# Kernel optimization log

Measured on AMD Instinct MI355X. Metric: run time of the kernel, lower is better.

The kernel has to match this reference:

```python
import jax, jax.numpy as jnp
import numpy as np

IN_CAPS, OUT_CAPS, OUT_DIM = 32, 10, 16


def squash(s):
    # s: [B, out_caps, out_dim]
    sq = jnp.sum(s * s, axis=2)              # [B, out_caps]
    mod = jnp.sqrt(sq)
    scale = sq / (1.0 + sq) / mod            # matches torch: sqrmod/(1+sqrmod)/mod
    return scale[..., None] * s


def setup_inputs() -> dict:
    key = jax.random.key(0)
    k1, k2 = jax.random.split(key)
    B, in_dim = 4096, 288
    caps_output = jax.random.normal(k1, (B, IN_CAPS, in_dim), dtype=jnp.float32)
    # W initialized uniform(-1/32, 1/32) in the original; scale randn similarly small
    W = jax.random.uniform(k2, (IN_CAPS, in_dim, OUT_CAPS * OUT_DIM),
                           dtype=jnp.float32, minval=-1.0 / 32, maxval=1.0 / 32)
    b = jnp.zeros((IN_CAPS, OUT_CAPS), dtype=jnp.float32)
    return {"caps_output": caps_output, "W": W, "b": b}


def reference(caps_output, W, b):
    B = caps_output.shape[0]
    # caps_output.unsqueeze(2).matmul(W): per-input-capsule matmul
    u = jnp.einsum('bni,nio->bno', caps_output, W)          # [B, 32, 160]
    u = u.reshape(B, IN_CAPS, OUT_CAPS, OUT_DIM)            # [B, 32, 10, 16]

    c = jax.nn.softmax(b, axis=1)                           # [32, 10]
    s = jnp.einsum('no,bnod->bod', c, u)                    # [B, 10, 16]
    v = squash(s)

    b_batch = jnp.broadcast_to(b, (B, IN_CAPS, OUT_CAPS))
    for _ in range(3):
        # agreement: <u_predict, v>
        b_batch = b_batch + jnp.einsum('bnod,bod->bno', u, v)
        c = jax.nn.softmax(b_batch, axis=-1)                # [B, 32, 10]
        s = jnp.einsum('bno,bnod->bod', c, u)
        v = squash(s)
    return v
```

## Files before the change

kernel.cpp:

```cpp
#include <hip/hip_runtime.h>
#include <hip/hip_bf16.h>

#define IN_CAPS 32
#define OUT_CAPS 10
#define NOUT 160
#define KDIM 288
#define BATCH 4096
#define KSTEPS 9
#define CTILES 10
#define STR2 162

typedef __bf16 bf16x8 __attribute__((ext_vector_type(8)));
typedef float  f32x4  __attribute__((ext_vector_type(4)));
typedef __attribute__((address_space(1))) void as1_t;
typedef __attribute__((address_space(3))) void as3_t;

__global__ __launch_bounds__(256) void prep_w(const float* __restrict__ W,
                                              __bf16* __restrict__ Wf) {
    int f = blockIdx.x * 256 + threadIdx.x;
    int j    = f & 7;
    int l    = (f >> 3) & 63;
    int rest = f >> 9;
    int c    = rest % CTILES;
    int tnk  = rest / CTILES;
    int ks   = tnk % KSTEPS;
    int n    = tnk / KSTEPS;
    int k    = ks * 32 + (l >> 4) * 8 + j;
    int col  = c * 16 + (l & 15);
    Wf[f] = (__bf16)W[(n * KDIM + k) * NOUT + col];
}

__global__ __launch_bounds__(256) void gemm_u(const float* __restrict__ caps,
                                              const __bf16* __restrict__ Wf,
                                              uint4* __restrict__ up) {
    __shared__ float abuf[3][64 * 32];

    const int n    = blockIdx.y;
    const int rb   = blockIdx.x;
    const int w    = threadIdx.x >> 6;
    const int lane = threadIdx.x & 63;
    const int lm   = lane & 15;
    const int lk   = lane >> 4;

    const int s0 = w * 128 + lane;
    const int s1 = s0 + 64;
    const int r0 = s0 >> 3;
    const int r1 = s1 >> 3;
    const int c0 = (s0 & 7) ^ (r0 & 7);
    const int c1 = (s1 & 7) ^ (r1 & 7);
    const float* g0 = caps + (size_t)(rb * 64 + r0) * (IN_CAPS * KDIM) + n * KDIM + c0 * 4;
    const float* g1 = caps + (size_t)(rb * 64 + r1) * (IN_CAPS * KDIM) + n * KDIM + c1 * 4;

    f32x4 acc[CTILES];
#pragma unroll
    for (int ct = 0; ct < CTILES; ++ct) acc[ct] = (f32x4){0.f, 0.f, 0.f, 0.f};

    const int rloc = w * 16 + lm;
    const int h0   = ((lk * 2)     ^ (lm & 7)) * 4;
    const int h1   = ((lk * 2 + 1) ^ (lm & 7)) * 4;
    const __bf16* wfn = Wf + (size_t)n * (KSTEPS * CTILES * 512) + lane * 8;

    __builtin_amdgcn_global_load_lds((const as1_t*)g0, (as3_t*)&abuf[0][w * 512],       16, 0, 0);
    __builtin_amdgcn_global_load_lds((const as1_t*)g1, (as3_t*)&abuf[0][w * 512 + 256], 16, 0, 0);
    __builtin_amdgcn_global_load_lds((const as1_t*)(g0 + 32), (as3_t*)&abuf[1][w * 512],       16, 0, 0);
    __builtin_amdgcn_global_load_lds((const as1_t*)(g1 + 32), (as3_t*)&abuf[1][w * 512 + 256], 16, 0, 0);

#pragma unroll
    for (int ks = 0; ks < KSTEPS; ++ks) {
        if (ks + 1 < KSTEPS) asm volatile("s_waitcnt vmcnt(2)" ::: "memory");
        else                 asm volatile("s_waitcnt vmcnt(0)" ::: "memory");

        const float* bc = abuf[ks % 3];
        f32x4 x0 = *(const f32x4*)&bc[rloc * 32 + h0];
        f32x4 x1 = *(const f32x4*)&bc[rloc * 32 + h1];
        bf16x8 a;
        a[0] = (__bf16)x0[0]; a[1] = (__bf16)x0[1];
        a[2] = (__bf16)x0[2]; a[3] = (__bf16)x0[3];
        a[4] = (__bf16)x1[0]; a[5] = (__bf16)x1[1];
        a[6] = (__bf16)x1[2]; a[7] = (__bf16)x1[3];

        const __bf16* wks = wfn + (size_t)ks * (CTILES * 512);
#pragma unroll
        for (int ct = 0; ct < CTILES; ++ct) {
            bf16x8 bfr = *(const bf16x8*)(wks + ct * 512);
            acc[ct] = __builtin_amdgcn_mfma_f32_16x16x32_bf16(a, bfr, acc[ct], 0, 0, 0);
        }

        if (ks + 2 < KSTEPS) {
            float* dst = &abuf[(ks + 2) % 3][0];
            __builtin_amdgcn_global_load_lds((const as1_t*)(g0 + (ks + 2) * 32),
                                             (as3_t*)(dst + w * 512),       16, 0, 0);
            __builtin_amdgcn_global_load_lds((const as1_t*)(g1 + (ks + 2) * 32),
                                             (as3_t*)(dst + w * 512 + 256), 16, 0, 0);
        }
    }

    const int rw = rb * 2 + (w >> 1);
    const int mt = w & 1;
    const size_t cbase = ((((size_t)n * 128 + rw) * 2 + mt) * 5) * 64 + lane;
#pragma unroll
    for (int p = 0; p < 5; ++p) {
        bf16x8 pk;
#pragma unroll
        for (int j = 0; j < 8; ++j)
            pk[j] = (__bf16)acc[2 * p + (j >> 2)][j & 3];
        up[cbase + (size_t)p * 64] = __builtin_bit_cast(uint4, pk);
    }
}

__global__ __launch_bounds__(256) void routing(const uint4* __restrict__ up,
                                               const float* __restrict__ bbias,
                                               float* __restrict__ out) {
    __shared__ __bf16 ul[4][IN_CAPS * STR2];
    __shared__ float  bl[4][IN_CAPS * OUT_CAPS];
    __shared__ float  cs[4][IN_CAPS * OUT_CAPS];
    __shared__ float  ss[4][NOUT];
    __shared__ float  vs[4][NOUT];
    __shared__ float  scale_s[4][16];

    const int t  = threadIdx.x;
    const int b0 = blockIdx.x * 4;
    const int rw = b0 >> 5;
    const int mt = (b0 >> 4) & 1;
    const int lk = (b0 >> 2) & 3;

    for (int c = t; c < 2560; c += 256) {
        int n   = c / 80;
        int rem = c - n * 80;
        int p   = rem >> 4;
        int lm  = rem & 15;
        size_t idx = ((((size_t)n * 128 + rw) * 2 + mt) * 5 + p) * 64 + lk * 16 + lm;
        bf16x8 v = __builtin_bit_cast(bf16x8, up[idx]);
#pragma unroll
        for (int j = 0; j < 8; ++j) {
            int ct = 2 * p + (j >> 2);
            int rr = j & 3;
            ul[rr][n * STR2 + ct * 16 + lm] = v[j];
        }
    }
    const int grp = t >> 6;
    const int g   = t & 63;
    for (int pp = g; pp < IN_CAPS * OUT_CAPS; pp += 64) bl[grp][pp] = bbias[pp];
    __syncthreads();

    for (int it = 0; it < 4; ++it) {
        if (it > 0) {
            for (int pp = g; pp < IN_CAPS * OUT_CAPS; pp += 64) {
                int n = pp & 31;
                int o = pp >> 5;
                float a = 0.f;
#pragma unroll
                for (int d = 0; d < 16; ++d)
                    a += (float)ul[grp][n * STR2 + o * 16 + d] * vs[grp][o * 16 + d];
                bl[grp][n * 10 + o] += a;
            }
            __syncthreads();
        }
        if (g < IN_CAPS) {
            float m = bl[grp][g * 10];
#pragma unroll
            for (int o = 1; o < 10; ++o) m = fmaxf(m, bl[grp][g * 10 + o]);
            float e[10];
            float sum = 0.f;
#pragma unroll
            for (int o = 0; o < 10; ++o) { e[o] = __expf(bl[grp][g * 10 + o] - m); sum += e[o]; }
            float inv = 1.0f / sum;
#pragma unroll
            for (int o = 0; o < 10; ++o) cs[grp][g * 10 + o] = e[o] * inv;
        }
        __syncthreads();
        for (int p = g; p < NOUT; p += 64) {
            int o = p >> 4;
            float a = 0.f;
#pragma unroll
            for (int nn = 0; nn < IN_CAPS; ++nn)
                a += cs[grp][nn * 10 + o] * (float)ul[grp][nn * STR2 + p];
            ss[grp][p] = a;
        }
        __syncthreads();
        if (g < OUT_CAPS) {
            float sq = 0.f;
#pragma unroll
            for (int d = 0; d < 16; ++d) { float x = ss[grp][g * 16 + d]; sq += x * x; }
            scale_s[grp][g] = sq / ((1.0f + sq) * sqrtf(sq));
        }
        __syncthreads();
        for (int p = g; p < NOUT; p += 64) vs[grp][p] = scale_s[grp][p >> 4] * ss[grp][p];
        __syncthreads();
    }

    for (int p = g; p < NOUT; p += 64)
        out[(size_t)(b0 + grp) * NOUT + p] = vs[grp][p];
}

extern "C" void kernel_launch(void* const* d_in, const int* in_sizes, int n_in,
                              void* d_out, int out_size, void* d_ws, size_t ws_size,
                              hipStream_t stream) {
    const float* caps  = (const float*)d_in[0];
    const float* W     = (const float*)d_in[1];
    const float* bbias = (const float*)d_in[2];
    float* out = (float*)d_out;

    __bf16* Wf = (__bf16*)d_ws;
    uint4*  up = (uint4*)((char*)d_ws + 2949120);

    prep_w<<<dim3(5760), dim3(256), 0, stream>>>(W, Wf);
    gemm_u<<<dim3(64, 32), dim3(256), 0, stream>>>(caps, Wf, up);
    routing<<<dim3(BATCH / 4), dim3(256), 0, stream>>>(up, bbias, out);
}
```

Before: 86.61 us.

## Stage W tiles in LDS shared across waves with double-buffered barriers

In the GEMM kernel, the per-wave direct global loads of the bf16 W fragments are replaced by cooperative async global-to-LDS copies. All four waves now read W from one shared LDS tile instead of each re-fetching it from cache. The activation pipeline drops from triple buffering with vmcnt-based waits to double buffering with a block barrier every K step. This cuts redundant W traffic but adds a barrier per step and shortens the prefetch distance for the caps stream.

```diff
diff --git a/kernel.cpp b/kernel.cpp
--- a/kernel.cpp
+++ b/kernel.cpp
@@ -33,7 +33,8 @@
 __global__ __launch_bounds__(256) void gemm_u(const float* __restrict__ caps,
                                               const __bf16* __restrict__ Wf,
                                               uint4* __restrict__ up) {
-    __shared__ float abuf[3][64 * 32];
+    __shared__ float  As[2][64 * 32];
+    __shared__ __bf16 Bs[2][5120];
 
     const int n    = blockIdx.y;
     const int rb   = blockIdx.x;
@@ -42,57 +43,63 @@
     const int lm   = lane & 15;
     const int lk   = lane >> 4;
 
-    const int s0 = w * 128 + lane;
-    const int s1 = s0 + 64;
-    const int r0 = s0 >> 3;
-    const int r1 = s1 >> 3;
-    const int c0 = (s0 & 7) ^ (r0 & 7);
-    const int c1 = (s1 & 7) ^ (r1 & 7);
-    const float* g0 = caps + (size_t)(rb * 64 + r0) * (IN_CAPS * KDIM) + n * KDIM + c0 * 4;
-    const float* g1 = caps + (size_t)(rb * 64 + r1) * (IN_CAPS * KDIM) + n * KDIM + c1 * 4;
+    const int sl0 = w * 128 + lane;
+    const int sl1 = sl0 + 64;
+    const int r0 = sl0 >> 3, r1 = sl1 >> 3;
+    const int c0 = (sl0 & 7) ^ (r0 & 7);
+    const int c1 = (sl1 & 7) ^ (r1 & 7);
+    const float* ga0 = caps + ((size_t)(rb * 64 + r0) * IN_CAPS + n) * KDIM + c0 * 4;
+    const float* ga1 = caps + ((size_t)(rb * 64 + r1) * IN_CAPS + n) * KDIM + c1 * 4;
+
+    const __bf16* wb = Wf + (size_t)n * (KSTEPS * 5120);
+
+#define STAGE(ks, buf) do {                                                          \
+    __builtin_amdgcn_global_load_lds((const as1_t*)(ga0 + (ks) * 32),                \
+                                     (as3_t*)&As[buf][w * 512],        16, 0, 0);    \
+    __builtin_amdgcn_global_load_lds((const as1_t*)(ga1 + (ks) * 32),                \
+                                     (as3_t*)&As[buf][w * 512 + 256],  16, 0, 0);    \
+    __builtin_amdgcn_global_load_lds((const as1_t*)(wb + (size_t)(ks) * 5120 +       \
+                                     (w * 2) * 512 + lane * 8),                      \
+                                     (as3_t*)&Bs[buf][(w * 2) * 512],  16, 0, 0);    \
+    __builtin_amdgcn_global_load_lds((const as1_t*)(wb + (size_t)(ks) * 5120 +       \
+                                     (w * 2 + 1) * 512 + lane * 8),                  \
+                                     (as3_t*)&Bs[buf][(w * 2 + 1) * 512], 16, 0, 0); \
+    if (w < 2)                                                                       \
+        __builtin_amdgcn_global_load_lds((const as1_t*)(wb + (size_t)(ks) * 5120 +   \
+                                         (8 + w) * 512 + lane * 8),                  \
+                                         (as3_t*)&Bs[buf][(8 + w) * 512], 16, 0, 0); \
+} while (0)
 
     f32x4 acc[CTILES];
 #pragma unroll
     for (int ct = 0; ct < CTILES; ++ct) acc[ct] = (f32x4){0.f, 0.f, 0.f, 0.f};
 
-    const int rloc = w * 16 + lm;
-    const int h0   = ((lk * 2)     ^ (lm & 7)) * 4;
-    const int h1   = ((lk * 2 + 1) ^ (lm & 7)) * 4;
-    const __bf16* wfn = Wf + (size_t)n * (KSTEPS * CTILES * 512) + lane * 8;
-
-    __builtin_amdgcn_global_load_lds((const as1_t*)g0, (as3_t*)&abuf[0][w * 512],       16, 0, 0);
-    __builtin_amdgcn_global_load_lds((const as1_t*)g1, (as3_t*)&abuf[0][w * 512 + 256], 16, 0, 0);
-    __builtin_amdgcn_global_load_lds((const as1_t*)(g0 + 32), (as3_t*)&abuf[1][w * 512],       16, 0, 0);
-    __builtin_amdgcn_global_load_lds((const as1_t*)(g1 + 32), (as3_t*)&abuf[1][w * 512 + 256], 16, 0, 0);
-
-#pragma unroll
+    const int rl = w * 16 + lm;
+    const int h0 = ((2 * lk)     ^ (lm & 7)) * 4;
+    const int h1 = ((2 * lk + 1) ^ (lm & 7)) * 4;
+
+    STAGE(0, 0);
+    __syncthreads();
+
     for (int ks = 0; ks < KSTEPS; ++ks) {
-        if (ks + 1 < KSTEPS) asm volatile("s_waitcnt vmcnt(2)" ::: "memory");
-        else                 asm volatile("s_waitcnt vmcnt(0)" ::: "memory");
-
-        const float* bc = abuf[ks % 3];
-        f32x4 x0 = *(const f32x4*)&bc[rloc * 32 + h0];
-        f32x4 x1 = *(const f32x4*)&bc[rloc * 32 + h1];
+        if (ks + 1 < KSTEPS) STAGE(ks + 1, (ks + 1) & 1);
+
+        const float*  Ac = As[ks & 1];
+        const __bf16* Bc = Bs[ks & 1];
+        f32x4 x0 = *(const f32x4*)&Ac[rl * 32 + h0];
+        f32x4 x1 = *(const f32x4*)&Ac[rl * 32 + h1];
         bf16x8 a;
         a[0] = (__bf16)x0[0]; a[1] = (__bf16)x0[1];
         a[2] = (__bf16)x0[2]; a[3] = (__bf16)x0[3];
         a[4] = (__bf16)x1[0]; a[5] = (__bf16)x1[1];
         a[6] = (__bf16)x1[2]; a[7] = (__bf16)x1[3];
 
-        const __bf16* wks = wfn + (size_t)ks * (CTILES * 512);
 #pragma unroll
         for (int ct = 0; ct < CTILES; ++ct) {
-            bf16x8 bfr = *(const bf16x8*)(wks + ct * 512);
+            bf16x8 bfr = *(const bf16x8*)&Bc[ct * 512 + lane * 8];
             acc[ct] = __builtin_amdgcn_mfma_f32_16x16x32_bf16(a, bfr, acc[ct], 0, 0, 0);
         }
-
-        if (ks + 2 < KSTEPS) {
-            float* dst = &abuf[(ks + 2) % 3][0];
-            __builtin_amdgcn_global_load_lds((const as1_t*)(g0 + (ks + 2) * 32),
-                                             (as3_t*)(dst + w * 512),       16, 0, 0);
-            __builtin_amdgcn_global_load_lds((const as1_t*)(g1 + (ks + 2) * 32),
-                                             (as3_t*)(dst + w * 512 + 256), 16, 0, 0);
-        }
+        __syncthreads();
     }
 
     const int rw = rb * 2 + (w >> 1);
@@ -106,6 +113,7 @@
             pk[j] = (__bf16)acc[2 * p + (j >> 2)][j & 3];
         up[cbase + (size_t)p * 64] = __builtin_bit_cast(uint4, pk);
     }
+#undef STAGE
 }
 
 __global__ __launch_bounds__(256) void routing(const uint4* __restrict__ up,
```

After: 78.87 us. 8.9% less time.

## Preload full bf16 A tile into LDS, double-buffer W via LDS, reorder grid

Applied to the files above, without the earlier changes.

Each gemm_u block now loads its whole 64x288 slice of caps up front with vector loads. It converts the slice to bf16 and stores it in padded LDS, replacing the fp32 triple-buffered async pipeline. The W fragments are staged into an LDS double buffer with async global-to-LDS loads, with a barrier after each k-step. The grid is flattened so that the 32 input-capsule blocks sharing a row block are scheduled next to each other, which is meant to improve DRAM locality on the contiguous caps rows. In exchange, the A load is no longer overlapped with MFMA work, and per-step barriers plus larger LDS use may lower occupancy.

```diff
diff --git a/kernel.cpp b/kernel.cpp
--- a/kernel.cpp
+++ b/kernel.cpp
@@ -9,6 +9,7 @@
 #define KSTEPS 9
 #define CTILES 10
 #define STR2 162
+#define APAD 296
 
 typedef __bf16 bf16x8 __attribute__((ext_vector_type(8)));
 typedef float  f32x4  __attribute__((ext_vector_type(4)));
@@ -33,66 +34,72 @@
 __global__ __launch_bounds__(256) void gemm_u(const float* __restrict__ caps,
                                               const __bf16* __restrict__ Wf,
                                               uint4* __restrict__ up) {
-    __shared__ float abuf[3][64 * 32];
-
-    const int n    = blockIdx.y;
-    const int rb   = blockIdx.x;
-    const int w    = threadIdx.x >> 6;
-    const int lane = threadIdx.x & 63;
+    __shared__ __bf16 As[64 * APAD];
+    __shared__ __bf16 Bs[2][5120];
+
+    const int lin  = blockIdx.x;
+    const int n    = lin & 31;
+    const int rb   = lin >> 5;
+    const int t    = threadIdx.x;
+    const int w    = t >> 6;
+    const int lane = t & 63;
     const int lm   = lane & 15;
     const int lk   = lane >> 4;
 
-    const int s0 = w * 128 + lane;
-    const int s1 = s0 + 64;
-    const int r0 = s0 >> 3;
-    const int r1 = s1 >> 3;
-    const int c0 = (s0 & 7) ^ (r0 & 7);
-    const int c1 = (s1 & 7) ^ (r1 & 7);
-    const float* g0 = caps + (size_t)(rb * 64 + r0) * (IN_CAPS * KDIM) + n * KDIM + c0 * 4;
-    const float* g1 = caps + (size_t)(rb * 64 + r1) * (IN_CAPS * KDIM) + n * KDIM + c1 * 4;
+    const __bf16* wb = Wf + (size_t)n * (KSTEPS * 5120);
+#define STAGE_B(ks, buf) do {                                                         \
+    const __bf16* _s = wb + (size_t)(ks) * 5120;                                      \
+    __builtin_amdgcn_global_load_lds((const as1_t*)(_s + t * 8),                      \
+                                     (as3_t*)&Bs[buf][t * 8],         16, 0, 0);      \
+    __builtin_amdgcn_global_load_lds((const as1_t*)(_s + (t + 256) * 8),              \
+                                     (as3_t*)&Bs[buf][(t + 256) * 8], 16, 0, 0);      \
+    if (t < 128)                                                                      \
+        __builtin_amdgcn_global_load_lds((const as1_t*)(_s + (t + 512) * 8),          \
+                                         (as3_t*)&Bs[buf][(t + 512) * 8], 16, 0, 0);  \
+} while (0)
+
+    const float* abase = caps + ((size_t)rb * 64 * IN_CAPS + n) * KDIM;
+    f32x4 raw[9][2];
+#pragma unroll
+    for (int i = 0; i < 9; ++i) {
+        int c = t + i * 256;
+        int row = c / 36, pp = c - row * 36;
+        const float* src = abase + (size_t)row * (IN_CAPS * KDIM) + pp * 8;
+        raw[i][0] = *(const f32x4*)src;
+        raw[i][1] = *(const f32x4*)(src + 4);
+    }
+    STAGE_B(0, 0);
+#pragma unroll
+    for (int i = 0; i < 9; ++i) {
+        int c = t + i * 256;
+        int row = c / 36, pp = c - row * 36;
+        bf16x8 v;
+#pragma unroll
+        for (int j = 0; j < 4; ++j) {
+            v[j]     = (__bf16)raw[i][0][j];
+            v[j + 4] = (__bf16)raw[i][1][j];
+        }
+        *(bf16x8*)&As[row * APAD + pp * 8] = v;
+    }
 
     f32x4 acc[CTILES];
 #pragma unroll
     for (int ct = 0; ct < CTILES; ++ct) acc[ct] = (f32x4){0.f, 0.f, 0.f, 0.f};
 
-    const int rloc = w * 16 + lm;
-    const int h0   = ((lk * 2)     ^ (lm & 7)) * 4;
-    const int h1   = ((lk * 2 + 1) ^ (lm & 7)) * 4;
-    const __bf16* wfn = Wf + (size_t)n * (KSTEPS * CTILES * 512) + lane * 8;
-
-    __builtin_amdgcn_global_load_lds((const as1_t*)g0, (as3_t*)&abuf[0][w * 512],       16, 0, 0);
-    __builtin_amdgcn_global_load_lds((const as1_t*)g1, (as3_t*)&abuf[0][w * 512 + 256], 16, 0, 0);
-    __builtin_amdgcn_global_load_lds((const as1_t*)(g0 + 32), (as3_t*)&abuf[1][w * 512],       16, 0, 0);
-    __builtin_amdgcn_global_load_lds((const as1_t*)(g1 + 32), (as3_t*)&abuf[1][w * 512 + 256], 16, 0, 0);
-
+    __syncthreads();
+
+    const __bf16* arow = &As[(w * 16 + lm) * APAD];
 #pragma unroll
     for (int ks = 0; ks < KSTEPS; ++ks) {
-        if (ks + 1 < KSTEPS) asm volatile("s_waitcnt vmcnt(2)" ::: "memory");
-        else                 asm volatile("s_waitcnt vmcnt(0)" ::: "memory");
-
-        const float* bc = abuf[ks % 3];
-        f32x4 x0 = *(const f32x4*)&bc[rloc * 32 + h0];
-        f32x4 x1 = *(const f32x4*)&bc[rloc * 32 + h1];
-        bf16x8 a;
-        a[0] = (__bf16)x0[0]; a[1] = (__bf16)x0[1];
-        a[2] = (__bf16)x0[2]; a[3] = (__bf16)x0[3];
-        a[4] = (__bf16)x1[0]; a[5] = (__bf16)x1[1];
-        a[6] = (__bf16)x1[2]; a[7] = (__bf16)x1[3];
-
-        const __bf16* wks = wfn + (size_t)ks * (CTILES * 512);
+        if (ks + 1 < KSTEPS) STAGE_B(ks + 1, (ks + 1) & 1);
+        bf16x8 a = *(const bf16x8*)(arow + ks * 32 + lk * 8);
+        const __bf16* Bc = &Bs[ks & 1][lane * 8];
 #pragma unroll
         for (int ct = 0; ct < CTILES; ++ct) {
-            bf16x8 bfr = *(const bf16x8*)(wks + ct * 512);
+            bf16x8 bfr = *(const bf16x8*)(Bc + ct * 512);
             acc[ct] = __builtin_amdgcn_mfma_f32_16x16x32_bf16(a, bfr, acc[ct], 0, 0, 0);
         }
-
-        if (ks + 2 < KSTEPS) {
-            float* dst = &abuf[(ks + 2) % 3][0];
-            __builtin_amdgcn_global_load_lds((const as1_t*)(g0 + (ks + 2) * 32),
-                                             (as3_t*)(dst + w * 512),       16, 0, 0);
-            __builtin_amdgcn_global_load_lds((const as1_t*)(g1 + (ks + 2) * 32),
-                                             (as3_t*)(dst + w * 512 + 256), 16, 0, 0);
-        }
+        __syncthreads();
     }
 
     const int rw = rb * 2 + (w >> 1);
@@ -106,6 +113,7 @@
             pk[j] = (__bf16)acc[2 * p + (j >> 2)][j & 3];
         up[cbase + (size_t)p * 64] = __builtin_bit_cast(uint4, pk);
     }
+#undef STAGE_B
 }
 
 __global__ __launch_bounds__(256) void routing(const uint4* __restrict__ up,
@@ -205,6 +213,6 @@
     uint4*  up = (uint4*)((char*)d_ws + 2949120);
 
     prep_w<<<dim3(5760), dim3(256), 0, stream>>>(W, Wf);
-    gemm_u<<<dim3(64, 32), dim3(256), 0, stream>>>(caps, Wf, up);
+    gemm_u<<<dim3(2048), dim3(256), 0, stream>>>(caps, Wf, up);
     routing<<<dim3(BATCH / 4), dim3(256), 0, stream>>>(up, bbias, out);
 }
```

Result: slower. 90.69 us (+4.7%).
